# Performance work log

Hardware: AMD Instinct MI355X
Metric: run time of the kernel (lower is better)

Reference implementation:

```python
import jax, jax.numpy as jnp
import numpy as np

LN_EPS = 1e-5


def _layernorm(x, w, b):
    mu = jnp.mean(x, axis=-1, keepdims=True)
    var = jnp.mean((x - mu) ** 2, axis=-1, keepdims=True)
    return (x - mu) * jax.lax.rsqrt(var + LN_EPS) * w + b


def setup_inputs() -> dict:
    key = jax.random.key(0)
    n, d = 512, 256
    ks = jax.random.split(key, 12)
    s = 1.0 / np.sqrt(d)
    inp = {
        "h": jax.random.normal(ks[0], (n, d), dtype=jnp.float32),
        "e": jax.random.normal(ks[1], (n, n, d), dtype=jnp.float32),
        "t_emb": jax.random.normal(ks[2], (d,), dtype=jnp.float32),
        "W1": jax.random.uniform(ks[3], (d, d), jnp.float32, -s, s),
        "W2": jax.random.uniform(ks[4], (d, d), jnp.float32, -s, s),
        "W3": jax.random.uniform(ks[5], (d, d), jnp.float32, -s, s),
        "W_t": jax.random.uniform(ks[6], (d, d), jnp.float32, -s, s),
        "W4": jax.random.uniform(ks[7], (d, d), jnp.float32, -s, s),
        "W5": jax.random.uniform(ks[8], (d, d), jnp.float32, -s, s),
        "gate_w": jax.random.uniform(ks[9], (d, 1), jnp.float32, -s, s),
        "gate_b": jax.random.uniform(ks[10], (1,), jnp.float32, -s, s),
        "ln_e_w": jnp.ones((d,), jnp.float32),
        "ln_e_b": jnp.zeros((d,), jnp.float32),
        "ln_h_w": jnp.ones((d,), jnp.float32),
        "ln_h_b": jnp.zeros((d,), jnp.float32),
    }
    return inp


def reference(h, e, t_emb, W1, W2, W3, W_t, W4, W5, gate_w, gate_b,
              ln_e_w, ln_e_b, ln_h_w, ln_h_b):
    # nn.Linear applies x @ W.T (no bias except gate)
    t_bias = t_emb @ W_t.T                      # (d,)
    hi = (h @ W1.T)[:, None, :]                 # (n,1,d)
    hj = (h @ W2.T)[None, :, :]                 # (1,n,d)
    pre = hi + hj + jnp.einsum('ijd,kd->ijk', e, W3) + t_bias  # (n,n,d)
    e_new = jax.nn.relu(_layernorm(pre, ln_e_w, ln_e_b))       # (n,n,d)
    logits = e_new @ gate_w + gate_b            # (n,n,1)
    eta = jax.nn.softmax(logits, axis=1)        # softmax over j (dim=1)
    agg = jnp.einsum('ijk,ijd,kd->ik', eta * 1.0, e_new, W5) if False else \
          jnp.sum(eta * jnp.einsum('ijd,kd->ijk', e_new, W5), axis=1)  # (n,d)
    h_new = h + jax.nn.relu(_layernorm(h @ W4.T + agg, ln_h_w, ln_h_b))
    return (h_new, e_new)
```

## Files before the change

kernel.cpp:

```cpp
#include <hip/hip_runtime.h>

#define NN 512
#define DD 256

typedef float f32x4 __attribute__((ext_vector_type(4)));
typedef short s16x8 __attribute__((ext_vector_type(8)));

__device__ __forceinline__ unsigned short f2bf(float f) {
    unsigned u = __float_as_uint(f);
    u += 0x7fffu + ((u >> 16) & 1u);
    return (unsigned short)(u >> 16);
}
__device__ __forceinline__ float bf2f(unsigned short s) {
    return __uint_as_float(((unsigned)s) << 16);
}

__global__ __launch_bounds__(256) void k1_pre(
    const float* __restrict__ h,  const float* __restrict__ W1,
    const float* __restrict__ W2, const float* __restrict__ W4,
    const float* __restrict__ t_emb, const float* __restrict__ W_t,
    const float* __restrict__ W3,
    float* __restrict__ hb, float* __restrict__ hW2, float* __restrict__ hW4,
    unsigned short* __restrict__ w3b,
    float* __restrict__ wacc, float* __restrict__ zacc)
{
    __shared__ float xs[8][DD];
    __shared__ float st[DD];
    const int b = blockIdx.x;
    const int t = threadIdx.x;
    if (b < 64) {
        #pragma unroll
        for (int r = 0; r < 8; ++r) xs[r][t] = h[(size_t)(b * 8 + r) * DD + t];
        st[t] = t_emb[t];
        __syncthreads();
        float a1[8], a2[8], a4[8];
        #pragma unroll
        for (int r = 0; r < 8; ++r) { a1[r] = 0.f; a2[r] = 0.f; a4[r] = 0.f; }
        float tb = 0.f;
        for (int d = 0; d < DD; ++d) {
            const float w1 = W1[(size_t)t * DD + d];
            const float w2 = W2[(size_t)t * DD + d];
            const float w4 = W4[(size_t)t * DD + d];
            tb = fmaf(st[d], W_t[(size_t)t * DD + d], tb);
            #pragma unroll
            for (int r = 0; r < 8; ++r) {
                const float x = xs[r][d];
                a1[r] = fmaf(x, w1, a1[r]);
                a2[r] = fmaf(x, w2, a2[r]);
                a4[r] = fmaf(x, w4, a4[r]);
            }
        }
        #pragma unroll
        for (int r = 0; r < 8; ++r) {
            const size_t o = (size_t)(b * 8 + r) * DD + t;
            hb[o] = a1[r] + tb; hW2[o] = a2[r]; hW4[o] = a4[r];
        }
    } else if (b == 64) {
        for (int c = t; c < DD * DD / 4; c += 256) {
            const f32x4 v = *reinterpret_cast<const f32x4*>(W3 + (size_t)c * 4);
            const unsigned lo = ((unsigned)f2bf(v[1]) << 16) | f2bf(v[0]);
            const unsigned hi = ((unsigned)f2bf(v[3]) << 16) | f2bf(v[2]);
            *reinterpret_cast<uint2*>(w3b + (size_t)c * 4) = make_uint2(lo, hi);
        }
    } else {
        const f32x4 zero = (f32x4){0.f, 0.f, 0.f, 0.f};
        for (int c = t; c < NN * DD / 4; c += 256)
            *reinterpret_cast<f32x4*>(wacc + (size_t)c * 4) = zero;
        if (t < 256) { zacc[t] = 0.f; zacc[t + 256] = 0.f; }
    }
}

__global__ __launch_bounds__(256) void k2_big(
    const float* __restrict__ e,
    const unsigned short* __restrict__ w3b,
    const float* __restrict__ hb, const float* __restrict__ hW2,
    const float* __restrict__ gate_w, const float* __restrict__ gate_b,
    const float* __restrict__ ln_e_w, const float* __restrict__ ln_e_b,
    float* __restrict__ out_e,
    float* __restrict__ wacc, float* __restrict__ zacc)
{
    const int b = blockIdx.x;
    const int row_base = b * 32;
    const int i = row_base >> 9;
    const int tid = threadIdx.x;
    const int w = tid >> 6;
    const int l = tid & 63;
    const int l15 = l & 15;
    const int lg = l >> 4;

    __shared__ __align__(16) unsigned char sBuf[32 * 260 * 4];
    __shared__ unsigned short s_hbu[DD];
    __shared__ float s_lnw[DD], s_lnb[DD], s_gw[DD];
    __shared__ float s_part[32][4][2];
    __shared__ float s_glog[32][4];
    float* const sOut = (float*)sBuf;

    const float* esrc = e + (size_t)row_base * DD;
    f32x4 av[8];
    #pragma unroll
    for (int s = 0; s < 8; ++s)
        av[s] = *reinterpret_cast<const f32x4*>(esrc + (size_t)(s * 256 + tid) * 4);

    const unsigned short* bp = w3b + (size_t)(w * 64 + l15) * DD + lg * 8;
    s16x8 bb[4][4];
    #pragma unroll
    for (int kk = 0; kk < 4; ++kk)
        #pragma unroll
        for (int n = 0; n < 4; ++n)
            bb[kk][n] = *reinterpret_cast<const s16x8*>(bp + (size_t)n * 16 * DD + kk * 32);

    const float gb = gate_b[0];
    s_lnw[tid] = ln_e_w[tid];
    s_lnb[tid] = ln_e_b[tid];
    s_gw[tid]  = gate_w[tid];
    s_hbu[tid] = f2bf(hb[(size_t)i * DD + tid]);

    #pragma unroll
    for (int s = 0; s < 8; ++s) {
        const int flat = s * 256 + tid;
        const int r = flat >> 6;
        const int c4 = (flat & 63) * 4;
        const f32x4 v = av[s];
        const unsigned lo = ((unsigned)f2bf(v[1]) << 16) | f2bf(v[0]);
        const unsigned hi = ((unsigned)f2bf(v[3]) << 16) | f2bf(v[2]);
        const unsigned byte = ((unsigned)(r * 512 + c4 * 2)) ^ ((unsigned)(r & 7) << 4);
        *reinterpret_cast<uint2*>(sBuf + byte) = make_uint2(lo, hi);
    }
    __syncthreads();

    f32x4 acc[2][4];
    #pragma unroll
    for (int m = 0; m < 2; ++m)
        #pragma unroll
        for (int n = 0; n < 4; ++n)
            acc[m][n] = (f32x4){0.f, 0.f, 0.f, 0.f};

    const unsigned aswz = ((unsigned)(l15 & 7) << 4);
    #pragma unroll
    for (int kk = 0; kk < 8; ++kk) {
        s16x8 afr[2];
        #pragma unroll
        for (int m = 0; m < 2; ++m) {
            const unsigned byte = ((unsigned)((m * 16 + l15) * 512 + kk * 64 + lg * 16)) ^ aswz;
            afr[m] = *reinterpret_cast<const s16x8*>(sBuf + byte);
        }
        #pragma unroll
        for (int n = 0; n < 4; ++n)
            #pragma unroll
            for (int m = 0; m < 2; ++m)
                acc[m][n] = __builtin_amdgcn_mfma_f32_16x16x32_bf16(afr[m], bb[kk & 3][n], acc[m][n], 0, 0, 0);
        if (kk < 4) {
            #pragma unroll
            for (int n = 0; n < 4; ++n)
                bb[kk & 3][n] = *reinterpret_cast<const s16x8*>(bp + (size_t)n * 16 * DD + (kk + 4) * 32);
        }
    }

    float hbn[4];
    #pragma unroll
    for (int n = 0; n < 4; ++n) hbn[n] = bf2f(s_hbu[w * 64 + n * 16 + l15]);

    #pragma unroll
    for (int m = 0; m < 2; ++m) {
        #pragma unroll
        for (int q = 0; q < 4; ++q) {
            const int r = m * 16 + lg * 4 + q;
            const int j = (row_base + r) & 511;
            const float* h2p = hW2 + (size_t)j * DD + w * 64 + l15;
            float s1 = 0.f, s2 = 0.f;
            #pragma unroll
            for (int n = 0; n < 4; ++n) {
                const float v = acc[m][n][q] + hbn[n] + h2p[n * 16];
                acc[m][n][q] = v;
                s1 += v;
                s2 = fmaf(v, v, s2);
            }
            #pragma unroll
            for (int s = 1; s < 16; s <<= 1) {
                s1 += __shfl_xor(s1, s, 64);
                s2 += __shfl_xor(s2, s, 64);
            }
            if (l15 == 0) { s_part[r][w][0] = s1; s_part[r][w][1] = s2; }
        }
    }
    __syncthreads();

    #pragma unroll
    for (int m = 0; m < 2; ++m) {
        #pragma unroll
        for (int q = 0; q < 4; ++q) {
            const int r = m * 16 + lg * 4 + q;
            float S1 = 0.f, S2 = 0.f;
            #pragma unroll
            for (int ww = 0; ww < 4; ++ww) { S1 += s_part[r][ww][0]; S2 += s_part[r][ww][1]; }
            const float mu = S1 * (1.f / 256.f);
            const float rs = rsqrtf(S2 * (1.f / 256.f) - mu * mu + 1e-5f);
            float gl = 0.f;
            #pragma unroll
            for (int n = 0; n < 4; ++n) {
                const int c = w * 64 + n * 16 + l15;
                float v = (acc[m][n][q] - mu) * rs * s_lnw[c] + s_lnb[c];
                v = fmaxf(v, 0.f);
                acc[m][n][q] = v;
                sOut[r * 260 + c] = v;
                gl = fmaf(v, s_gw[c], gl);
            }
            #pragma unroll
            for (int s = 1; s < 16; s <<= 1) gl += __shfl_xor(gl, s, 64);
            if (l15 == 0) s_glog[r][w] = gl;
        }
    }
    __syncthreads();

    float p[4] = {0.f, 0.f, 0.f, 0.f};
    float zl = 0.f;
    #pragma unroll
    for (int m = 0; m < 2; ++m) {
        #pragma unroll
        for (int q = 0; q < 4; ++q) {
            const int r = m * 16 + lg * 4 + q;
            const float lv = gb + s_glog[r][0] + s_glog[r][1] + s_glog[r][2] + s_glog[r][3];
            const float ex = __expf(lv);
            zl += ex;
            #pragma unroll
            for (int n = 0; n < 4; ++n) p[n] = fmaf(ex, acc[m][n][q], p[n]);
        }
    }
    #pragma unroll
    for (int n = 0; n < 4; ++n) {
        p[n] += __shfl_xor(p[n], 16, 64);
        p[n] += __shfl_xor(p[n], 32, 64);
    }
    zl += __shfl_xor(zl, 16, 64);
    zl += __shfl_xor(zl, 32, 64);
    if (lg == 0) {
        #pragma unroll
        for (int n = 0; n < 4; ++n)
            atomicAdd(&wacc[(size_t)i * DD + w * 64 + n * 16 + l15], p[n]);
    }
    if (w == 0 && l == 0) atomicAdd(&zacc[i], zl);

    #pragma unroll
    for (int s = 0; s < 8; ++s) {
        const int ch = s * 256 + tid;
        const int r = ch >> 6;
        const int c4 = (ch & 63) * 4;
        const f32x4 v = *reinterpret_cast<const f32x4*>(&sOut[r * 260 + c4]);
        *reinterpret_cast<f32x4*>(out_e + (size_t)(row_base + r) * DD + c4) = v;
    }
}

__global__ __launch_bounds__(256) void k4_final(
    const float* __restrict__ wacc, const float* __restrict__ zacc,
    const float* __restrict__ W5,
    const float* __restrict__ hW4, const float* __restrict__ h,
    const float* __restrict__ ln_h_w, const float* __restrict__ ln_h_b,
    float* __restrict__ out_h)
{
    const int i = blockIdx.x;
    const int k = threadIdx.x;
    __shared__ float xs[DD];
    __shared__ float red[256];

    const float zinv = 1.f / zacc[i];
    xs[k] = wacc[(size_t)i * DD + k] * zinv;
    __syncthreads();
    float a = 0.f;
    for (int d = 0; d < DD; ++d) a = fmaf(xs[d], W5[(size_t)k * DD + d], a);
    const float p = hW4[(size_t)i * DD + k] + a;

    red[k] = p;
    __syncthreads();
    for (int s = 128; s > 0; s >>= 1) {
        if (k < s) red[k] += red[k + s];
        __syncthreads();
    }
    const float mu = red[0] * (1.f / 256.f);
    __syncthreads();
    const float d0 = p - mu;
    red[k] = d0 * d0;
    __syncthreads();
    for (int s = 128; s > 0; s >>= 1) {
        if (k < s) red[k] += red[k + s];
        __syncthreads();
    }
    const float rs = rsqrtf(red[0] * (1.f / 256.f) + 1e-5f);
    float v = d0 * rs * ln_h_w[k] + ln_h_b[k];
    v = fmaxf(v, 0.f);
    out_h[(size_t)i * DD + k] = h[(size_t)i * DD + k] + v;
}

extern "C" void kernel_launch(void* const* d_in, const int* in_sizes, int n_in,
                              void* d_out, int out_size, void* d_ws, size_t ws_size,
                              hipStream_t stream)
{
    const float* h      = (const float*)d_in[0];
    const float* e      = (const float*)d_in[1];
    const float* t_emb  = (const float*)d_in[2];
    const float* W1     = (const float*)d_in[3];
    const float* W2     = (const float*)d_in[4];
    const float* W3     = (const float*)d_in[5];
    const float* W_t    = (const float*)d_in[6];
    const float* W4     = (const float*)d_in[7];
    const float* W5     = (const float*)d_in[8];
    const float* gate_w = (const float*)d_in[9];
    const float* gate_b = (const float*)d_in[10];
    const float* ln_e_w = (const float*)d_in[11];
    const float* ln_e_b = (const float*)d_in[12];
    const float* ln_h_w = (const float*)d_in[13];
    const float* ln_h_b = (const float*)d_in[14];

    float* out_h = (float*)d_out;
    float* out_e = out_h + NN * DD;

    float* wsf  = (float*)d_ws;
    float* hb   = wsf;
    float* hW2  = hb + NN * DD;
    float* hW4  = hW2 + NN * DD;
    float* wacc = hW4 + NN * DD;
    float* zacc = wacc + NN * DD;
    unsigned short* w3b = (unsigned short*)(zacc + NN);

    k1_pre<<<66, 256, 0, stream>>>(h, W1, W2, W4, t_emb, W_t, W3,
                                   hb, hW2, hW4, w3b, wacc, zacc);
    k2_big<<<8192, 256, 0, stream>>>(e, w3b, hb, hW2, gate_w, gate_b,
                                     ln_e_w, ln_e_b, out_e, wacc, zacc);
    k4_final<<<512, 256, 0, stream>>>(wacc, zacc, W5, hW4, h,
                                      ln_h_w, ln_h_b, out_h);
}
```

Before: 284.5 us.

## Load e tile directly to LDS as fp32 and store out_e straight from registers

Replaces the register-staged global load and in-register bf16 conversion of the e tile with direct global-to-LDS loads (global_load_lds) of fp32 data, stored in swizzled order. The bf16 packing moves to the MFMA operand read from LDS. The LDS-staged coalesced writeback of out_e is dropped, and each lane now writes its normalized values to global memory directly. This cuts register pressure and staging overhead, but the out_e stores become scattered 4-byte writes (16 contiguous floats per row per n), which may hurt write coalescing. LDS traffic per MFMA operand also doubles.

Measured after the change: 282.5 us. About the same (-0.7%).

```diff
diff --git a/kernel.cpp b/kernel.cpp
--- a/kernel.cpp
+++ b/kernel.cpp
@@ -13,6 +13,22 @@
 }
 __device__ __forceinline__ float bf2f(unsigned short s) {
     return __uint_as_float(((unsigned)s) << 16);
+}
+__device__ __forceinline__ unsigned packbf(float a, float b) {
+    return ((unsigned)f2bf(b) << 16) | f2bf(a);
+}
+__device__ __forceinline__ s16x8 pack_bf(const f32x4 v0, const f32x4 v1) {
+    s16x8 a;
+    a[0] = (short)f2bf(v0[0]); a[1] = (short)f2bf(v0[1]);
+    a[2] = (short)f2bf(v0[2]); a[3] = (short)f2bf(v0[3]);
+    a[4] = (short)f2bf(v1[0]); a[5] = (short)f2bf(v1[1]);
+    a[6] = (short)f2bf(v1[2]); a[7] = (short)f2bf(v1[3]);
+    return a;
+}
+__device__ __forceinline__ void gl_lds16(const float* g, float* lds) {
+    __builtin_amdgcn_global_load_lds(
+        (const __attribute__((address_space(1))) void*)g,
+        (__attribute__((address_space(3))) void*)lds, 16, 0, 0);
 }
 
 __global__ __launch_bounds__(256) void k1_pre(
@@ -58,9 +74,8 @@
     } else if (b == 64) {
         for (int c = t; c < DD * DD / 4; c += 256) {
             const f32x4 v = *reinterpret_cast<const f32x4*>(W3 + (size_t)c * 4);
-            const unsigned lo = ((unsigned)f2bf(v[1]) << 16) | f2bf(v[0]);
-            const unsigned hi = ((unsigned)f2bf(v[3]) << 16) | f2bf(v[2]);
-            *reinterpret_cast<uint2*>(w3b + (size_t)c * 4) = make_uint2(lo, hi);
+            *reinterpret_cast<uint2*>(w3b + (size_t)c * 4) =
+                make_uint2(packbf(v[0], v[1]), packbf(v[2], v[3]));
         }
     } else {
         const f32x4 zero = (f32x4){0.f, 0.f, 0.f, 0.f};
@@ -88,18 +103,20 @@
     const int l15 = l & 15;
     const int lg = l >> 4;
 
-    __shared__ __align__(16) unsigned char sBuf[32 * 260 * 4];
+    __shared__ __align__(16) float sAf[32 * 256];
     __shared__ unsigned short s_hbu[DD];
     __shared__ float s_lnw[DD], s_lnb[DD], s_gw[DD];
     __shared__ float s_part[32][4][2];
     __shared__ float s_glog[32][4];
-    float* const sOut = (float*)sBuf;
-
-    const float* esrc = e + (size_t)row_base * DD;
-    f32x4 av[8];
-    #pragma unroll
-    for (int s = 0; s < 8; ++s)
-        av[s] = *reinterpret_cast<const f32x4*>(esrc + (size_t)(s * 256 + tid) * 4);
+
+    {
+        const float* esrc = e + (size_t)row_base * DD;
+        #pragma unroll
+        for (int t = 0; t < 8; ++t) {
+            const int r = w * 8 + t;
+            gl_lds16(esrc + (size_t)r * DD + ((l ^ (r & 7)) << 2), sAf + r * 256);
+        }
+    }
 
     const unsigned short* bp = w3b + (size_t)(w * 64 + l15) * DD + lg * 8;
     s16x8 bb[4][4];
@@ -114,18 +131,6 @@
     s_lnb[tid] = ln_e_b[tid];
     s_gw[tid]  = gate_w[tid];
     s_hbu[tid] = f2bf(hb[(size_t)i * DD + tid]);
-
-    #pragma unroll
-    for (int s = 0; s < 8; ++s) {
-        const int flat = s * 256 + tid;
-        const int r = flat >> 6;
-        const int c4 = (flat & 63) * 4;
-        const f32x4 v = av[s];
-        const unsigned lo = ((unsigned)f2bf(v[1]) << 16) | f2bf(v[0]);
-        const unsigned hi = ((unsigned)f2bf(v[3]) << 16) | f2bf(v[2]);
-        const unsigned byte = ((unsigned)(r * 512 + c4 * 2)) ^ ((unsigned)(r & 7) << 4);
-        *reinterpret_cast<uint2*>(sBuf + byte) = make_uint2(lo, hi);
-    }
     __syncthreads();
 
     f32x4 acc[2][4];
@@ -135,14 +140,18 @@
         for (int n = 0; n < 4; ++n)
             acc[m][n] = (f32x4){0.f, 0.f, 0.f, 0.f};
 
-    const unsigned aswz = ((unsigned)(l15 & 7) << 4);
     #pragma unroll
     for (int kk = 0; kk < 8; ++kk) {
         s16x8 afr[2];
         #pragma unroll
         for (int m = 0; m < 2; ++m) {
-            const unsigned byte = ((unsigned)((m * 16 + l15) * 512 + kk * 64 + lg * 16)) ^ aswz;
-            afr[m] = *reinterpret_cast<const s16x8*>(sBuf + byte);
+            const int r = m * 16 + l15;
+            const int c0 = kk * 8 + lg * 2;
+            const int s0 = c0 ^ (r & 7);
+            const int s1 = (c0 + 1) ^ (r & 7);
+            const f32x4 v0 = *reinterpret_cast<const f32x4*>(sAf + r * 256 + s0 * 4);
+            const f32x4 v1 = *reinterpret_cast<const f32x4*>(sAf + r * 256 + s1 * 4);
+            afr[m] = pack_bf(v0, v1);
         }
         #pragma unroll
         for (int n = 0; n < 4; ++n)
@@ -195,6 +204,7 @@
             for (int ww = 0; ww < 4; ++ww) { S1 += s_part[r][ww][0]; S2 += s_part[r][ww][1]; }
             const float mu = S1 * (1.f / 256.f);
             const float rs = rsqrtf(S2 * (1.f / 256.f) - mu * mu + 1e-5f);
+            const size_t rowg = (size_t)(row_base + r);
             float gl = 0.f;
             #pragma unroll
             for (int n = 0; n < 4; ++n) {
@@ -202,7 +212,7 @@
                 float v = (acc[m][n][q] - mu) * rs * s_lnw[c] + s_lnb[c];
                 v = fmaxf(v, 0.f);
                 acc[m][n][q] = v;
-                sOut[r * 260 + c] = v;
+                out_e[rowg * DD + c] = v;
                 gl = fmaf(v, s_gw[c], gl);
             }
             #pragma unroll
@@ -239,15 +249,6 @@
             atomicAdd(&wacc[(size_t)i * DD + w * 64 + n * 16 + l15], p[n]);
     }
     if (w == 0 && l == 0) atomicAdd(&zacc[i], zl);
-
-    #pragma unroll
-    for (int s = 0; s < 8; ++s) {
-        const int ch = s * 256 + tid;
-        const int r = ch >> 6;
-        const int c4 = (ch & 63) * 4;
-        const f32x4 v = *reinterpret_cast<const f32x4*>(&sOut[r * 260 + c4]);
-        *reinterpret_cast<f32x4*>(out_e + (size_t)(row_base + r) * DD + c4) = v;
-    }
 }
 
 __global__ __launch_bounds__(256) void k4_final(
```
